# Kernel tuning notes

Measured on AMD Instinct MI355X. Metric: run time of the kernel, lower is better.

## Reference

```python
import jax, jax.numpy as jnp
import numpy as np

N = 500000
B = 128  # number of segments (graphs)
IN_DIM = 256
KEY_DIM = 100
K = 8        # num_group
VAL_DIM = 32  # embedding_dim // K


def setup_inputs() -> dict:
    key = jax.random.key(0)
    ks = jax.random.split(key, 8)
    x = jax.random.normal(ks[0], (N, IN_DIM), dtype=jnp.float32)
    batch = jnp.sort(jax.random.randint(ks[1], (N,), 0, B)).astype(jnp.int64)
    s = 0.05
    Wk = jax.random.normal(ks[2], (KEY_DIM, IN_DIM), dtype=jnp.float32) * s
    bk = jax.random.normal(ks[3], (KEY_DIM,), dtype=jnp.float32) * s
    Wq = jax.random.normal(ks[4], (K, KEY_DIM), dtype=jnp.float32) * s
    bq = jax.random.normal(ks[5], (K,), dtype=jnp.float32) * s
    Wv = jax.random.normal(ks[6], (VAL_DIM, IN_DIM), dtype=jnp.float32) * s
    bv = jax.random.normal(ks[7], (VAL_DIM,), dtype=jnp.float32) * s
    return {"x": x, "batch": batch, "Wk": Wk, "bk": bk, "Wq": Wq, "bq": bq, "Wv": Wv, "bv": bv}


def segment_softmax(w, seg, num_segments):
    # softmax over rows within each segment, independently per column (dim=0 in torch)
    m = jax.ops.segment_max(w, seg, num_segments=num_segments)   # [B, k]
    e = jnp.exp(w - m[seg])                                      # [N, k]
    s = jax.ops.segment_sum(e, seg, num_segments=num_segments)   # [B, k]
    return e / s[seg]


def reference(x, batch, Wk, bk, Wq, bq, Wv, bv):
    seg = batch.astype(jnp.int32)
    # 1x1 Conv2d on [N, C, 1, 1] == linear layer on [N, C]
    key = x @ Wk.T + bk                 # [N, key_dim]
    val = x @ Wv.T + bv                 # [N, val_dim]
    weights = key @ Wq.T + bq           # [N, k]
    norm_w = segment_softmax(weights, seg, B)            # [N, k]
    # embs[b] = norm_w[seg==b].T @ val[seg==b]  -> [B, k, val_dim]
    embs = jax.ops.segment_sum(norm_w[:, :, None] * val[:, None, :], seg, num_segments=B)
    return embs, norm_w
```

## Files before the change

kernel.cpp:

```cpp
#include <hip/hip_runtime.h>


#define NSEG 128
#define KQ 8
#define VD 32
#define NOUT 40
#define INDIM 256
#define ROWS 128
#define CCH 32
#define XSTR 36
#define ESTR 12
#define VSTR 36
#define SMEMF (ROWS * (ESTR + VSTR))

__global__ __launch_bounds__(256) void k_setup(
    const float* __restrict__ Wk, const float* __restrict__ bk,
    const float* __restrict__ Wq, const float* __restrict__ bq,
    const float* __restrict__ Wv, const float* __restrict__ bv,
    float* __restrict__ WO, float* __restrict__ bo,
    float* __restrict__ segsum, float* __restrict__ embs) {
    int b = blockIdx.x;
    int c = threadIdx.x;
    if (b < NOUT) {
        if (b < KQ) {
            float a = 0.f;
            for (int j = 0; j < 100; ++j) a = fmaf(Wq[b * 100 + j], Wk[j * INDIM + c], a);
            WO[b * INDIM + c] = a;
            if (c == 0) {
                float s = bq[b];
                for (int j = 0; j < 100; ++j) s = fmaf(Wq[b * 100 + j], bk[j], s);
                bo[b] = s;
            }
        } else {
            int v = b - KQ;
            WO[b * INDIM + c] = Wv[v * INDIM + c];
            if (c == 0) bo[b] = bv[v];
        }
    } else {
        int i = (b - NOUT) * 256 + c;
        if (i < NSEG * KQ * VD) {
            embs[i] = 0.f;
        } else {
            int j = i - NSEG * KQ * VD;
            if (j < NSEG * KQ) segsum[j] = 0.f;
        }
    }
}

__global__ __launch_bounds__(ROWS, 3) void k_main(
    const float* __restrict__ x, const int* __restrict__ batch,
    const float* __restrict__ WO, const float* __restrict__ bo,
    float* __restrict__ eout,
    float* __restrict__ segsum, float* __restrict__ embs, int N) {
    __shared__ float smem[SMEMF];
    __shared__ int sg[ROWS];
    const int tid = threadIdx.x;
    const int row0 = blockIdx.x * ROWS;
    const int row = row0 + tid;
    const bool valid = row < N;

    sg[tid] = valid ? batch[row] : batch[N - 1];

    float acc[NOUT];
#pragma unroll
    for (int o = 0; o < NOUT; ++o) acc[o] = bo[o];

    float* xs = smem;
    for (int cc = 0; cc < INDIM; cc += CCH) {
        __syncthreads();
#pragma unroll
        for (int i = 0; i < ROWS * CCH / 4 / ROWS; ++i) {
            int g = i * ROWS + tid;
            int r = g >> 3;
            int c = (g & 7) << 2;
            float4 v = make_float4(0.f, 0.f, 0.f, 0.f);
            int rr = row0 + r;
            if (rr < N) v = *(const float4*)&x[(size_t)rr * INDIM + cc + c];
            *(float4*)&xs[r * XSTR + c] = v;
        }
        __syncthreads();
#pragma unroll
        for (int c4 = 0; c4 < CCH; c4 += 4) {
            float4 xv = *(const float4*)&xs[tid * XSTR + c4];
            const float* wp = &WO[cc + c4];
#pragma unroll
            for (int o = 0; o < NOUT; ++o) {
                const float* w = wp + o * INDIM;
                acc[o] = fmaf(xv.x, w[0],
                         fmaf(xv.y, w[1],
                         fmaf(xv.z, w[2],
                         fmaf(xv.w, w[3], acc[o]))));
            }
        }
    }
    __syncthreads();

    float e[KQ];
#pragma unroll
    for (int k = 0; k < KQ; ++k) e[k] = valid ? expf(acc[k]) : 0.f;

    if (valid) {
        *(float4*)&eout[(size_t)row * KQ]     = make_float4(e[0], e[1], e[2], e[3]);
        *(float4*)&eout[(size_t)row * KQ + 4] = make_float4(e[4], e[5], e[6], e[7]);
    }

    float* es = smem;
    float* vs = smem + ROWS * ESTR;
    *(float4*)&es[tid * ESTR]     = make_float4(e[0], e[1], e[2], e[3]);
    *(float4*)&es[tid * ESTR + 4] = make_float4(e[4], e[5], e[6], e[7]);
#pragma unroll
    for (int i = 0; i < VD; i += 4) {
        float4 v = valid ? make_float4(acc[KQ + i], acc[KQ + i + 1],
                                       acc[KQ + i + 2], acc[KQ + i + 3])
                         : make_float4(0.f, 0.f, 0.f, 0.f);
        *(float4*)&vs[tid * VSTR + i] = v;
    }
    __syncthreads();

    const int k0 = tid >> 5;
    const int vcol = tid & 31;
    float a0 = 0.f, a1 = 0.f, s0 = 0.f, s1 = 0.f;
    int cur = sg[0];
    for (int r = 0; r < ROWS; ++r) {
        int s = sg[r];
        if (s != cur) {
            atomicAdd(&embs[cur * (KQ * VD) + k0 * VD + vcol], a0);
            atomicAdd(&embs[cur * (KQ * VD) + (k0 + 4) * VD + vcol], a1);
            if (vcol == 0) {
                atomicAdd(&segsum[cur * KQ + k0], s0);
                atomicAdd(&segsum[cur * KQ + k0 + 4], s1);
            }
            a0 = a1 = s0 = s1 = 0.f;
            cur = s;
        }
        float ev0 = es[r * ESTR + k0];
        float ev1 = es[r * ESTR + k0 + 4];
        float vvv = vs[r * VSTR + vcol];
        a0 = fmaf(ev0, vvv, a0);
        a1 = fmaf(ev1, vvv, a1);
        s0 += ev0;
        s1 += ev1;
    }
    atomicAdd(&embs[cur * (KQ * VD) + k0 * VD + vcol], a0);
    atomicAdd(&embs[cur * (KQ * VD) + (k0 + 4) * VD + vcol], a1);
    if (vcol == 0) {
        atomicAdd(&segsum[cur * KQ + k0], s0);
        atomicAdd(&segsum[cur * KQ + k0 + 4], s1);
    }
}

__global__ __launch_bounds__(256) void k_final(
    float* __restrict__ wnorm, const int* __restrict__ batch,
    const float* __restrict__ segsum, float* __restrict__ embs, int N) {
    int gid = blockIdx.x * 256 + threadIdx.x;
    if (gid < NSEG * KQ * VD) {
        embs[gid] = embs[gid] / segsum[gid >> 5];
    }
    if (gid < N) {
        int s = batch[gid];
        float4 e0 = *(float4*)&wnorm[(size_t)gid * KQ];
        float4 e1 = *(float4*)&wnorm[(size_t)gid * KQ + 4];
        const float* ss = &segsum[s * KQ];
        e0.x /= ss[0]; e0.y /= ss[1]; e0.z /= ss[2]; e0.w /= ss[3];
        e1.x /= ss[4]; e1.y /= ss[5]; e1.z /= ss[6]; e1.w /= ss[7];
        *(float4*)&wnorm[(size_t)gid * KQ]     = e0;
        *(float4*)&wnorm[(size_t)gid * KQ + 4] = e1;
    }
}

extern "C" void kernel_launch(void* const* d_in, const int* in_sizes, int n_in,
                              void* d_out, int out_size, void* d_ws, size_t ws_size,
                              hipStream_t stream) {
    const float* x   = (const float*)d_in[0];
    const int* batch = (const int*)d_in[1];
    const float* Wk  = (const float*)d_in[2];
    const float* bk  = (const float*)d_in[3];
    const float* Wq  = (const float*)d_in[4];
    const float* bq  = (const float*)d_in[5];
    const float* Wv  = (const float*)d_in[6];
    const float* bv  = (const float*)d_in[7];
    const int N = in_sizes[1];

    float* ws_f = (float*)d_ws;
    float* WO = ws_f;
    float* bo = ws_f + NOUT * INDIM;
    float* segsum = ws_f + NOUT * INDIM + NOUT + 8;

    float* embs  = (float*)d_out;
    float* wnorm = (float*)d_out + NSEG * KQ * VD;

    {
        int nb = NOUT + (NSEG * KQ * VD + NSEG * KQ + 255) / 256;
        k_setup<<<nb, 256, 0, stream>>>(Wk, bk, Wq, bq, Wv, bv, WO, bo, segsum, embs);
    }
    {
        int nb = (N + ROWS - 1) / ROWS;
        k_main<<<nb, ROWS, 0, stream>>>(x, batch, WO, bo, wnorm, segsum, embs, N);
    }
    {
        int nb = (N + 255) / 256;
        k_final<<<nb, 256, 0, stream>>>(wnorm, batch, segsum, embs, N);
    }
}
```

Before: 951.2 us.

## Double-buffer x tiles with register prefetch and use 256-row blocks

```diff
diff --git a/kernel.cpp b/kernel.cpp
--- a/kernel.cpp
+++ b/kernel.cpp
@@ -6,9 +6,10 @@
 #define VD 32
 #define NOUT 40
 #define INDIM 256
-#define ROWS 128
-#define CCH 32
-#define XSTR 36
+#define ROWS 256
+#define CCH 16
+#define NCH (INDIM / CCH)
+#define XSTR 20
 #define ESTR 12
 #define VSTR 36
 #define SMEMF (ROWS * (ESTR + VSTR))
@@ -65,23 +66,41 @@
 #pragma unroll
     for (int o = 0; o < NOUT; ++o) acc[o] = bo[o];
 
-    float* xs = smem;
-    for (int cc = 0; cc < INDIM; cc += CCH) {
-        __syncthreads();
-#pragma unroll
-        for (int i = 0; i < ROWS * CCH / 4 / ROWS; ++i) {
-            int g = i * ROWS + tid;
-            int r = g >> 3;
-            int c = (g & 7) << 2;
-            float4 v = make_float4(0.f, 0.f, 0.f, 0.f);
-            int rr = row0 + r;
-            if (rr < N) v = *(const float4*)&x[(size_t)rr * INDIM + cc + c];
-            *(float4*)&xs[r * XSTR + c] = v;
-        }
-        __syncthreads();
+    float* xsA = smem;
+    float* xsB = smem + ROWS * XSTR;
+    const int srl = tid >> 2;
+    const int sc = (tid & 3) << 2;
+
+    {
+        float4 st[4];
+#pragma unroll
+        for (int i = 0; i < 4; ++i) {
+            int rr = row0 + i * 64 + srl;
+            st[i] = (rr < N) ? *(const float4*)&x[(size_t)rr * INDIM + sc]
+                             : make_float4(0.f, 0.f, 0.f, 0.f);
+        }
+#pragma unroll
+        for (int i = 0; i < 4; ++i)
+            *(float4*)&xsA[(i * 64 + srl) * XSTR + sc] = st[i];
+    }
+    __syncthreads();
+
+    for (int ch = 0; ch < NCH; ++ch) {
+        float4 st[4];
+        const bool more = (ch + 1 < NCH);
+        if (more) {
+            const int ccn = (ch + 1) * CCH;
+#pragma unroll
+            for (int i = 0; i < 4; ++i) {
+                int rr = row0 + i * 64 + srl;
+                st[i] = (rr < N) ? *(const float4*)&x[(size_t)rr * INDIM + ccn + sc]
+                                 : make_float4(0.f, 0.f, 0.f, 0.f);
+            }
+        }
+        const int cc = ch * CCH;
 #pragma unroll
         for (int c4 = 0; c4 < CCH; c4 += 4) {
-            float4 xv = *(const float4*)&xs[tid * XSTR + c4];
+            float4 xv = *(const float4*)&xsA[tid * XSTR + c4];
             const float* wp = &WO[cc + c4];
 #pragma unroll
             for (int o = 0; o < NOUT; ++o) {
@@ -92,8 +111,14 @@
                          fmaf(xv.w, w[3], acc[o]))));
             }
         }
-    }
-    __syncthreads();
+        if (more) {
+#pragma unroll
+            for (int i = 0; i < 4; ++i)
+                *(float4*)&xsB[(i * 64 + srl) * XSTR + sc] = st[i];
+        }
+        __syncthreads();
+        float* t = xsA; xsA = xsB; xsB = t;
+    }
 
     float e[KQ];
 #pragma unroll
@@ -109,44 +134,29 @@
     *(float4*)&es[tid * ESTR]     = make_float4(e[0], e[1], e[2], e[3]);
     *(float4*)&es[tid * ESTR + 4] = make_float4(e[4], e[5], e[6], e[7]);
 #pragma unroll
-    for (int i = 0; i < VD; i += 4) {
-        float4 v = valid ? make_float4(acc[KQ + i], acc[KQ + i + 1],
-                                       acc[KQ + i + 2], acc[KQ + i + 3])
-                         : make_float4(0.f, 0.f, 0.f, 0.f);
-        *(float4*)&vs[tid * VSTR + i] = v;
-    }
+    for (int i = 0; i < VD; i += 4)
+        *(float4*)&vs[tid * VSTR + i] = make_float4(acc[KQ + i], acc[KQ + i + 1],
+                                                    acc[KQ + i + 2], acc[KQ + i + 3]);
     __syncthreads();
 
-    const int k0 = tid >> 5;
+    const int kk = tid >> 5;
     const int vcol = tid & 31;
-    float a0 = 0.f, a1 = 0.f, s0 = 0.f, s1 = 0.f;
+    float a0 = 0.f, s0 = 0.f;
     int cur = sg[0];
     for (int r = 0; r < ROWS; ++r) {
         int s = sg[r];
         if (s != cur) {
-            atomicAdd(&embs[cur * (KQ * VD) + k0 * VD + vcol], a0);
-            atomicAdd(&embs[cur * (KQ * VD) + (k0 + 4) * VD + vcol], a1);
-            if (vcol == 0) {
-                atomicAdd(&segsum[cur * KQ + k0], s0);
-                atomicAdd(&segsum[cur * KQ + k0 + 4], s1);
-            }
-            a0 = a1 = s0 = s1 = 0.f;
-            cur = s;
-        }
-        float ev0 = es[r * ESTR + k0];
-        float ev1 = es[r * ESTR + k0 + 4];
-        float vvv = vs[r * VSTR + vcol];
-        a0 = fmaf(ev0, vvv, a0);
-        a1 = fmaf(ev1, vvv, a1);
-        s0 += ev0;
-        s1 += ev1;
-    }
-    atomicAdd(&embs[cur * (KQ * VD) + k0 * VD + vcol], a0);
-    atomicAdd(&embs[cur * (KQ * VD) + (k0 + 4) * VD + vcol], a1);
-    if (vcol == 0) {
-        atomicAdd(&segsum[cur * KQ + k0], s0);
-        atomicAdd(&segsum[cur * KQ + k0 + 4], s1);
-    }
+            atomicAdd(&embs[cur * (KQ * VD) + tid], a0);
+            if (vcol == 0) atomicAdd(&segsum[cur * KQ + kk], s0);
+            a0 = 0.f; s0 = 0.f; cur = s;
+        }
+        float ev = es[r * ESTR + kk];
+        float vv = vs[r * VSTR + vcol];
+        a0 = fmaf(ev, vv, a0);
+        s0 += ev;
+    }
+    atomicAdd(&embs[cur * (KQ * VD) + tid], a0);
+    if (vcol == 0) atomicAdd(&segsum[cur * KQ + kk], s0);
 }
 
 __global__ __launch_bounds__(256) void k_final(
```

New measurement: 1.603 ms. 1.69x slower.
